# Kernel optimization log

Measured on AMD Instinct MI355X. Metric: run time of the kernel, lower is better.

Reference implementation:

```python
import jax, jax.numpy as jnp
import numpy as np

B, H, S, D = 4, 16, 2048, 64


def setup_inputs() -> dict:
    key = jax.random.key(0)
    kq, kk, kv = jax.random.split(key, 3)
    Q = jax.random.normal(kq, (B, H, S, D), dtype=jnp.float32)
    K = jax.random.normal(kk, (B, H, S, D), dtype=jnp.float32)
    V = jax.random.normal(kv, (B, H, S, D), dtype=jnp.float32)
    # causal mask, True = position is masked (torch.masked_fill semantics)
    mask = jnp.triu(jnp.ones((S, S), dtype=bool), k=1)[None, None, :, :]
    return {"Q": Q, "K": K, "V": V, "mask": mask}


def _custom_softmax(x):
    # Faithful to the source: subtract the GLOBAL max of the tensor,
    # then normalize by the row-sum of exps along the last dim.
    x = x - jnp.max(x)
    e = jnp.exp(x)
    return e / jnp.sum(e, axis=-1, keepdims=True)


def reference(Q, K, V, mask):
    head_dim = jnp.asarray(K.shape[-1], dtype=Q.dtype)
    # scores: [B, H, S_q, S_k]
    scores = jnp.einsum("bhqd,bhkd->bhqk", Q, K) / jnp.sqrt(head_dim)
    scores = jnp.where(mask, -jnp.inf, scores)
    attn = _custom_softmax(scores)
    # p_drop = 0.0 -> dropout branch skipped in original
    out = jnp.einsum("bhqk,bhkd->bhqd", attn, V)
    return out
```

## Files before the change

kernel.cpp:

```cpp
#include <hip/hip_runtime.h>

typedef float    f32x4 __attribute__((ext_vector_type(4)));
typedef _Float16 f16x8 __attribute__((ext_vector_type(8)));

constexpr int S_LEN = 2048;
constexpr int DIM   = 64;
constexpr int QBLK  = 128;
constexpr int KBLK  = 64;

__global__ __launch_bounds__(256, 2)
void fattn(const float* __restrict__ Q, const float* __restrict__ K,
           const float* __restrict__ V, float* __restrict__ Out)
{
    __shared__ _Float16 Ks[2][KBLK * DIM];
    __shared__ _Float16 Vt[2][DIM * KBLK];

    const int tid  = threadIdx.x;
    const int lane = tid & 63;
    const int wv   = tid >> 6;
    const int g    = lane >> 4;
    const int c    = lane & 15;

    const int id   = blockIdx.x;
    const int bh   = (id & 7) * 8 + ((id >> 3) >> 3);
    const int pair = (id >> 3) & 7;
    const size_t base = (size_t)bh * (S_LEN * DIM);

    const int krow = tid >> 3;
    const int kd0  = (tid & 7) * 8;

    const float* Kb = K + base;
    const float* Vb = V + base;

    f32x4 kreg[2][2];
    float vreg[2][8];

#define LOAD_KV(KT)                                                            \
    {                                                                          \
        const int ktb_ = (KT) * KBLK;                                          \
        _Pragma("unroll")                                                      \
        for (int sl = 0; sl < 2; ++sl) {                                       \
            const float* kp = Kb + (size_t)(ktb_ + krow + sl * 32) * DIM + kd0;\
            kreg[sl][0] = *(const f32x4*)kp;                                   \
            kreg[sl][1] = *(const f32x4*)(kp + 4);                             \
            const float* vp = Vb + (size_t)(ktb_ + sl * 32 + wv * 4) * DIM + lane; \
            _Pragma("unroll")                                                  \
            for (int mi = 0; mi < 8; ++mi)                                     \
                vreg[sl][mi] = vp[(size_t)((mi >> 2) * 16 + (mi & 3)) * DIM];  \
        }                                                                      \
    }

#define WRITE_KV(B)                                                            \
    {                                                                          \
        _Pragma("unroll")                                                      \
        for (int sl = 0; sl < 2; ++sl) {                                       \
            const int row = krow + sl * 32;                                    \
            f16x8 kb;                                                          \
            _Pragma("unroll")                                                  \
            for (int i = 0; i < 4; ++i) {                                      \
                kb[i]     = (_Float16)kreg[sl][0][i];                          \
                kb[i + 4] = (_Float16)kreg[sl][1][i];                          \
            }                                                                  \
            *(f16x8*)((char*)Ks[B] + row * 128 + ((kd0 * 2) ^ ((row & 7) << 4))) = kb; \
            f16x8 vb;                                                          \
            _Pragma("unroll")                                                  \
            for (int mi = 0; mi < 8; ++mi) vb[mi] = (_Float16)vreg[sl][mi];    \
            const int oct = wv + sl * 4;                                       \
            *(f16x8*)((char*)Vt[B] + lane * 128 + ((oct * 16) ^ ((lane & 7) << 4))) = vb; \
        }                                                                      \
    }

    #pragma unroll 1
    for (int seg = 0; seg < 2; ++seg) {
        const int qt    = seg ? pair : 15 - pair;
        const int qbase = qt * QBLK;
        const int qw    = qbase + wv * 32;
        const int nkt   = 2 * qt + 2;

        f16x8 qf[2][2];
        #pragma unroll
        for (int qh = 0; qh < 2; ++qh) {
            const float* qp = Q + base + (size_t)(qw + qh * 16 + c) * DIM + g * 8;
            #pragma unroll
            for (int dc = 0; dc < 2; ++dc) {
                const f32x4 f0 = *(const f32x4*)(qp + dc * 32);
                const f32x4 f1 = *(const f32x4*)(qp + dc * 32 + 4);
                f16x8 q;
                #pragma unroll
                for (int i = 0; i < 4; ++i) {
                    q[i]     = (_Float16)(f0[i] * 0.125f);
                    q[i + 4] = (_Float16)(f1[i] * 0.125f);
                }
                qf[dc][qh] = q;
            }
        }

        f32x4 o[4][2];
        #pragma unroll
        for (int dt = 0; dt < 4; ++dt)
            #pragma unroll
            for (int qh = 0; qh < 2; ++qh) o[dt][qh] = (f32x4){0.f, 0.f, 0.f, 0.f};
        float m[2] = {-INFINITY, -INFINITY};
        float l[2] = {0.f, 0.f};

        LOAD_KV(0)
        __syncthreads();
        WRITE_KV(0)
        LOAD_KV(1)
        __syncthreads();

        for (int kt = 0; kt < nkt; ++kt) {
            const int cur = kt & 1;
            const int ktb = kt * KBLK;
            if (kt + 1 < nkt) WRITE_KV(cur ^ 1)
            if (kt + 2 < nkt) LOAD_KV(kt + 2)

            if (ktb <= qw + 31) {
                f32x4 s[4][2];
                __builtin_amdgcn_s_setprio(1);
                #pragma unroll
                for (int ct = 0; ct < 4; ++ct) {
                    const int r = ct * 16 + c;
                    const char* kp = (const char*)Ks[cur] + r * 128;
                    const f16x8 kf0 = *(const f16x8*)(kp + ((g * 16)      ^ ((r & 7) << 4)));
                    const f16x8 kf1 = *(const f16x8*)(kp + ((64 + g * 16) ^ ((r & 7) << 4)));
                    #pragma unroll
                    for (int qh = 0; qh < 2; ++qh) {
                        f32x4 acc = (f32x4){0.f, 0.f, 0.f, 0.f};
                        acc = __builtin_amdgcn_mfma_f32_16x16x32_f16(kf0, qf[0][qh], acc, 0, 0, 0);
                        acc = __builtin_amdgcn_mfma_f32_16x16x32_f16(kf1, qf[1][qh], acc, 0, 0, 0);
                        s[ct][qh] = acc;
                    }
                }
                __builtin_amdgcn_s_setprio(0);

                if (ktb + KBLK - 1 > qw) {
                    #pragma unroll
                    for (int ct = 0; ct < 4; ++ct)
                        #pragma unroll
                        for (int qh = 0; qh < 2; ++qh)
                            #pragma unroll
                            for (int r = 0; r < 4; ++r)
                                if (ktb + ct * 16 + g * 4 + r > qw + qh * 16 + c)
                                    s[ct][qh][r] = -INFINITY;
                }

                float rm[2];
                #pragma unroll
                for (int qh = 0; qh < 2; ++qh) {
                    float v = s[0][qh][0];
                    #pragma unroll
                    for (int ct = 0; ct < 4; ++ct)
                        #pragma unroll
                        for (int r = 0; r < 4; ++r) v = fmaxf(v, s[ct][qh][r]);
                    v = fmaxf(v, __shfl_xor(v, 16));
                    v = fmaxf(v, __shfl_xor(v, 32));
                    rm[qh] = v;
                }
                const float need = fmaxf(rm[0] - m[0], rm[1] - m[1]);
                if (!__all(need <= 8.f)) {
                    #pragma unroll
                    for (int qh = 0; qh < 2; ++qh) {
                        const float mn = fmaxf(m[qh], rm[qh]);
                        const float sc = __expf(m[qh] - mn);
                        m[qh] = mn;
                        l[qh] *= sc;
                        #pragma unroll
                        for (int dt = 0; dt < 4; ++dt)
                            #pragma unroll
                            for (int r = 0; r < 4; ++r) o[dt][qh][r] *= sc;
                    }
                }
                float rs[2] = {0.f, 0.f};
                #pragma unroll
                for (int ct = 0; ct < 4; ++ct)
                    #pragma unroll
                    for (int qh = 0; qh < 2; ++qh)
                        #pragma unroll
                        for (int r = 0; r < 4; ++r) {
                            const float p = __expf(s[ct][qh][r] - m[qh]);
                            s[ct][qh][r] = p;
                            rs[qh] += p;
                        }
                #pragma unroll
                for (int qh = 0; qh < 2; ++qh) {
                    float v = rs[qh];
                    v += __shfl_xor(v, 16);
                    v += __shfl_xor(v, 32);
                    l[qh] += v;
                }

                f16x8 pa[2][2];
                #pragma unroll
                for (int qh = 0; qh < 2; ++qh)
                    #pragma unroll
                    for (int kc = 0; kc < 2; ++kc) {
                        f16x8 p;
                        #pragma unroll
                        for (int r = 0; r < 4; ++r) {
                            p[r]     = (_Float16)s[2 * kc][qh][r];
                            p[r + 4] = (_Float16)s[2 * kc + 1][qh][r];
                        }
                        pa[qh][kc] = p;
                    }

                __builtin_amdgcn_s_setprio(1);
                #pragma unroll
                for (int dt = 0; dt < 4; ++dt) {
                    const int dd = dt * 16 + c;
                    const char* vp = (const char*)Vt[cur] + dd * 128;
                    #pragma unroll
                    for (int kc = 0; kc < 2; ++kc) {
                        const f16x8 vf = *(const f16x8*)(vp +
                            ((kc * 64 + g * 16) ^ ((dd & 7) << 4)));
                        #pragma unroll
                        for (int qh = 0; qh < 2; ++qh)
                            o[dt][qh] = __builtin_amdgcn_mfma_f32_16x16x32_f16(
                                vf, pa[qh][kc], o[dt][qh], 0, 0, 0);
                    }
                }
                __builtin_amdgcn_s_setprio(0);
            }
            __syncthreads();
        }

        #pragma unroll
        for (int qh = 0; qh < 2; ++qh) {
            const float invl = 1.f / l[qh];
            const size_t qoff = base + (size_t)(qw + qh * 16 + c) * DIM;
            #pragma unroll
            for (int dt = 0; dt < 4; ++dt) {
                f32x4 ov;
                #pragma unroll
                for (int r = 0; r < 4; ++r) ov[r] = o[dt][qh][r] * invl;
                *(f32x4*)(Out + qoff + dt * 16 + g * 4) = ov;
            }
        }
    }
#undef LOAD_KV
#undef WRITE_KV
}

extern "C" void kernel_launch(void* const* d_in, const int* in_sizes, int n_in,
                              void* d_out, int out_size, void* d_ws, size_t ws_size,
                              hipStream_t stream)
{
    const float* Q = (const float*)d_in[0];
    const float* K = (const float*)d_in[1];
    const float* V = (const float*)d_in[2];
    float* Out = (float*)d_out;
    fattn<<<dim3(512), 256, 0, stream>>>(Q, K, V, Out);
}
```

Measured before the change: 73.83 us.

## Process paired causal Q tiles concurrently in 512-thread blocks; use exp2 softmax

Each block now has 8 waves. Waves 0-3 handle the heavy query tile and waves 4-7 handle the light mirrored tile, all sharing one K/V stream, so the two segments no longer run one after another. Every thread loads one K/V slice per tile instead of two, which halves per-thread staging registers. Q is prescaled by log2(e)/sqrt(D) so the softmax can use native exp2, and the rescale threshold is raised to match the log2 domain. The light-tile waves sit idle once they pass their causal range but still hit the barrier on every iteration, which adds imbalance and sync cost.

```diff
diff --git a/kernel.cpp b/kernel.cpp
--- a/kernel.cpp
+++ b/kernel.cpp
@@ -8,7 +8,10 @@
 constexpr int QBLK  = 128;
 constexpr int KBLK  = 64;
 
-__global__ __launch_bounds__(256, 2)
+#define QSCALE 0.1803368801111f
+#define THR    11.5f
+
+__global__ __launch_bounds__(512, 4)
 void fattn(const float* __restrict__ Q, const float* __restrict__ K,
            const float* __restrict__ V, float* __restrict__ Out)
 {
@@ -21,220 +24,207 @@
     const int g    = lane >> 4;
     const int c    = lane & 15;
 
-    const int id   = blockIdx.x;
-    const int bh   = (id & 7) * 8 + ((id >> 3) >> 3);
-    const int pair = (id >> 3) & 7;
+    const int id = blockIdx.x;
+    const int bh = (id >> 2) & 63;
+    const int p  = (id & 256) ? (7 - (id & 3)) : (id & 3);
+    const int qt_hi = 15 - p;
+    const int qt = (wv < 4) ? qt_hi : p;
+    const int qw = qt * QBLK + (wv & 3) * 32;
+    const int nkt = 2 * qt_hi + 2;
     const size_t base = (size_t)bh * (S_LEN * DIM);
+
+    f16x8 qf[2][2];
+    #pragma unroll
+    for (int qh = 0; qh < 2; ++qh) {
+        const float* qp = Q + base + (size_t)(qw + qh * 16 + c) * DIM + g * 8;
+        #pragma unroll
+        for (int dc = 0; dc < 2; ++dc) {
+            const f32x4 f0 = *(const f32x4*)(qp + dc * 32);
+            const f32x4 f1 = *(const f32x4*)(qp + dc * 32 + 4);
+            f16x8 q;
+            #pragma unroll
+            for (int i = 0; i < 4; ++i) {
+                q[i]     = (_Float16)(f0[i] * QSCALE);
+                q[i + 4] = (_Float16)(f1[i] * QSCALE);
+            }
+            qf[dc][qh] = q;
+        }
+    }
 
     const int krow = tid >> 3;
     const int kd0  = (tid & 7) * 8;
-
     const float* Kb = K + base;
     const float* Vb = V + base;
-
-    f32x4 kreg[2][2];
-    float vreg[2][8];
+    const int vk0 = (wv >> 2) * 32 + (wv & 3) * 4;
+
+    f32x4 kreg[2];
+    float vreg[8];
 
 #define LOAD_KV(KT)                                                            \
     {                                                                          \
         const int ktb_ = (KT) * KBLK;                                          \
+        const float* kp = Kb + (size_t)(ktb_ + krow) * DIM + kd0;              \
+        kreg[0] = *(const f32x4*)kp;                                           \
+        kreg[1] = *(const f32x4*)(kp + 4);                                     \
+        const float* vp = Vb + (size_t)(ktb_ + vk0) * DIM + lane;              \
         _Pragma("unroll")                                                      \
-        for (int sl = 0; sl < 2; ++sl) {                                       \
-            const float* kp = Kb + (size_t)(ktb_ + krow + sl * 32) * DIM + kd0;\
-            kreg[sl][0] = *(const f32x4*)kp;                                   \
-            kreg[sl][1] = *(const f32x4*)(kp + 4);                             \
-            const float* vp = Vb + (size_t)(ktb_ + sl * 32 + wv * 4) * DIM + lane; \
-            _Pragma("unroll")                                                  \
-            for (int mi = 0; mi < 8; ++mi)                                     \
-                vreg[sl][mi] = vp[(size_t)((mi >> 2) * 16 + (mi & 3)) * DIM];  \
-        }                                                                      \
+        for (int mi = 0; mi < 8; ++mi)                                         \
+            vreg[mi] = vp[(size_t)((mi >> 2) * 16 + (mi & 3)) * DIM];          \
     }
 
 #define WRITE_KV(B)                                                            \
     {                                                                          \
+        f16x8 kb;                                                              \
         _Pragma("unroll")                                                      \
-        for (int sl = 0; sl < 2; ++sl) {                                       \
-            const int row = krow + sl * 32;                                    \
-            f16x8 kb;                                                          \
-            _Pragma("unroll")                                                  \
-            for (int i = 0; i < 4; ++i) {                                      \
-                kb[i]     = (_Float16)kreg[sl][0][i];                          \
-                kb[i + 4] = (_Float16)kreg[sl][1][i];                          \
-            }                                                                  \
-            *(f16x8*)((char*)Ks[B] + row * 128 + ((kd0 * 2) ^ ((row & 7) << 4))) = kb; \
-            f16x8 vb;                                                          \
-            _Pragma("unroll")                                                  \
-            for (int mi = 0; mi < 8; ++mi) vb[mi] = (_Float16)vreg[sl][mi];    \
-            const int oct = wv + sl * 4;                                       \
-            *(f16x8*)((char*)Vt[B] + lane * 128 + ((oct * 16) ^ ((lane & 7) << 4))) = vb; \
+        for (int i = 0; i < 4; ++i) {                                          \
+            kb[i]     = (_Float16)kreg[0][i];                                  \
+            kb[i + 4] = (_Float16)kreg[1][i];                                  \
         }                                                                      \
-    }
-
-    #pragma unroll 1
-    for (int seg = 0; seg < 2; ++seg) {
-        const int qt    = seg ? pair : 15 - pair;
-        const int qbase = qt * QBLK;
-        const int qw    = qbase + wv * 32;
-        const int nkt   = 2 * qt + 2;
-
-        f16x8 qf[2][2];
+        *(f16x8*)((char*)Ks[B] + krow * 128 + ((kd0 * 2) ^ ((krow & 7) << 4))) = kb; \
+        f16x8 vb;                                                              \
+        _Pragma("unroll")                                                      \
+        for (int mi = 0; mi < 8; ++mi) vb[mi] = (_Float16)vreg[mi];            \
+        *(f16x8*)((char*)Vt[B] + lane * 128 + ((wv * 16) ^ ((lane & 7) << 4))) = vb; \
+    }
+
+    f32x4 o[4][2];
+    #pragma unroll
+    for (int dt = 0; dt < 4; ++dt)
         #pragma unroll
-        for (int qh = 0; qh < 2; ++qh) {
-            const float* qp = Q + base + (size_t)(qw + qh * 16 + c) * DIM + g * 8;
-            #pragma unroll
-            for (int dc = 0; dc < 2; ++dc) {
-                const f32x4 f0 = *(const f32x4*)(qp + dc * 32);
-                const f32x4 f1 = *(const f32x4*)(qp + dc * 32 + 4);
-                f16x8 q;
-                #pragma unroll
-                for (int i = 0; i < 4; ++i) {
-                    q[i]     = (_Float16)(f0[i] * 0.125f);
-                    q[i + 4] = (_Float16)(f1[i] * 0.125f);
-                }
-                qf[dc][qh] = q;
-            }
-        }
-
-        f32x4 o[4][2];
-        #pragma unroll
-        for (int dt = 0; dt < 4; ++dt)
-            #pragma unroll
-            for (int qh = 0; qh < 2; ++qh) o[dt][qh] = (f32x4){0.f, 0.f, 0.f, 0.f};
-        float m[2] = {-INFINITY, -INFINITY};
-        float l[2] = {0.f, 0.f};
-
-        LOAD_KV(0)
-        __syncthreads();
-        WRITE_KV(0)
-        LOAD_KV(1)
-        __syncthreads();
-
-        for (int kt = 0; kt < nkt; ++kt) {
-            const int cur = kt & 1;
-            const int ktb = kt * KBLK;
-            if (kt + 1 < nkt) WRITE_KV(cur ^ 1)
-            if (kt + 2 < nkt) LOAD_KV(kt + 2)
-
-            if (ktb <= qw + 31) {
-                f32x4 s[4][2];
-                __builtin_amdgcn_s_setprio(1);
-                #pragma unroll
-                for (int ct = 0; ct < 4; ++ct) {
-                    const int r = ct * 16 + c;
-                    const char* kp = (const char*)Ks[cur] + r * 128;
-                    const f16x8 kf0 = *(const f16x8*)(kp + ((g * 16)      ^ ((r & 7) << 4)));
-                    const f16x8 kf1 = *(const f16x8*)(kp + ((64 + g * 16) ^ ((r & 7) << 4)));
-                    #pragma unroll
-                    for (int qh = 0; qh < 2; ++qh) {
-                        f32x4 acc = (f32x4){0.f, 0.f, 0.f, 0.f};
-                        acc = __builtin_amdgcn_mfma_f32_16x16x32_f16(kf0, qf[0][qh], acc, 0, 0, 0);
-                        acc = __builtin_amdgcn_mfma_f32_16x16x32_f16(kf1, qf[1][qh], acc, 0, 0, 0);
-                        s[ct][qh] = acc;
-                    }
-                }
-                __builtin_amdgcn_s_setprio(0);
-
-                if (ktb + KBLK - 1 > qw) {
-                    #pragma unroll
-                    for (int ct = 0; ct < 4; ++ct)
-                        #pragma unroll
-                        for (int qh = 0; qh < 2; ++qh)
-                            #pragma unroll
-                            for (int r = 0; r < 4; ++r)
-                                if (ktb + ct * 16 + g * 4 + r > qw + qh * 16 + c)
-                                    s[ct][qh][r] = -INFINITY;
-                }
-
-                float rm[2];
+        for (int qh = 0; qh < 2; ++qh) o[dt][qh] = (f32x4){0.f, 0.f, 0.f, 0.f};
+    float m[2] = {-INFINITY, -INFINITY};
+    float l[2] = {0.f, 0.f};
+
+    LOAD_KV(0)
+    WRITE_KV(0)
+    LOAD_KV(1)
+    __syncthreads();
+
+    for (int kt = 0; kt < nkt; ++kt) {
+        const int cur = kt & 1;
+        const int ktb = kt * KBLK;
+        if (kt + 1 < nkt) WRITE_KV(cur ^ 1)
+        if (kt + 2 < nkt) LOAD_KV(kt + 2)
+
+        if (ktb <= qw + 31) {
+            f32x4 s[4][2];
+            __builtin_amdgcn_s_setprio(1);
+            #pragma unroll
+            for (int ct = 0; ct < 4; ++ct) {
+                const int r = ct * 16 + c;
+                const char* kp = (const char*)Ks[cur] + r * 128;
+                const f16x8 kf0 = *(const f16x8*)(kp + ((g * 16)      ^ ((r & 7) << 4)));
+                const f16x8 kf1 = *(const f16x8*)(kp + ((64 + g * 16) ^ ((r & 7) << 4)));
                 #pragma unroll
                 for (int qh = 0; qh < 2; ++qh) {
-                    float v = s[0][qh][0];
-                    #pragma unroll
-                    for (int ct = 0; ct < 4; ++ct)
-                        #pragma unroll
-                        for (int r = 0; r < 4; ++r) v = fmaxf(v, s[ct][qh][r]);
-                    v = fmaxf(v, __shfl_xor(v, 16));
-                    v = fmaxf(v, __shfl_xor(v, 32));
-                    rm[qh] = v;
-                }
-                const float need = fmaxf(rm[0] - m[0], rm[1] - m[1]);
-                if (!__all(need <= 8.f)) {
-                    #pragma unroll
-                    for (int qh = 0; qh < 2; ++qh) {
-                        const float mn = fmaxf(m[qh], rm[qh]);
-                        const float sc = __expf(m[qh] - mn);
-                        m[qh] = mn;
-                        l[qh] *= sc;
-                        #pragma unroll
-                        for (int dt = 0; dt < 4; ++dt)
-                            #pragma unroll
-                            for (int r = 0; r < 4; ++r) o[dt][qh][r] *= sc;
-                    }
-                }
-                float rs[2] = {0.f, 0.f};
+                    f32x4 acc = (f32x4){0.f, 0.f, 0.f, 0.f};
+                    acc = __builtin_amdgcn_mfma_f32_16x16x32_f16(kf0, qf[0][qh], acc, 0, 0, 0);
+                    acc = __builtin_amdgcn_mfma_f32_16x16x32_f16(kf1, qf[1][qh], acc, 0, 0, 0);
+                    s[ct][qh] = acc;
+                }
+            }
+            __builtin_amdgcn_s_setprio(0);
+
+            if (ktb + KBLK - 1 > qw) {
                 #pragma unroll
                 for (int ct = 0; ct < 4; ++ct)
                     #pragma unroll
                     for (int qh = 0; qh < 2; ++qh)
                         #pragma unroll
-                        for (int r = 0; r < 4; ++r) {
-                            const float p = __expf(s[ct][qh][r] - m[qh]);
-                            s[ct][qh][r] = p;
-                            rs[qh] += p;
-                        }
+                        for (int r = 0; r < 4; ++r)
+                            if (ktb + ct * 16 + g * 4 + r > qw + qh * 16 + c)
+                                s[ct][qh][r] = -INFINITY;
+            }
+
+            float rm[2];
+            #pragma unroll
+            for (int qh = 0; qh < 2; ++qh) {
+                float v = s[0][qh][0];
+                #pragma unroll
+                for (int ct = 0; ct < 4; ++ct)
+                    #pragma unroll
+                    for (int r = 0; r < 4; ++r) v = fmaxf(v, s[ct][qh][r]);
+                v = fmaxf(v, __shfl_xor(v, 16));
+                v = fmaxf(v, __shfl_xor(v, 32));
+                rm[qh] = v;
+            }
+            const float need = fmaxf(rm[0] - m[0], rm[1] - m[1]);
+            if (!__all(need <= THR)) {
                 #pragma unroll
                 for (int qh = 0; qh < 2; ++qh) {
-                    float v = rs[qh];
-                    v += __shfl_xor(v, 16);
-                    v += __shfl_xor(v, 32);
-                    l[qh] += v;
-                }
-
-                f16x8 pa[2][2];
+                    const float mn = fmaxf(m[qh], rm[qh]);
+                    const float sc = __builtin_amdgcn_exp2f(m[qh] - mn);
+                    m[qh] = mn;
+                    l[qh] *= sc;
+                    #pragma unroll
+                    for (int dt = 0; dt < 4; ++dt)
+                        #pragma unroll
+                        for (int r = 0; r < 4; ++r) o[dt][qh][r] *= sc;
+                }
+            }
+            float rs[2] = {0.f, 0.f};
+            #pragma unroll
+            for (int ct = 0; ct < 4; ++ct)
                 #pragma unroll
                 for (int qh = 0; qh < 2; ++qh)
                     #pragma unroll
-                    for (int kc = 0; kc < 2; ++kc) {
-                        f16x8 p;
-                        #pragma unroll
-                        for (int r = 0; r < 4; ++r) {
-                            p[r]     = (_Float16)s[2 * kc][qh][r];
-                            p[r + 4] = (_Float16)s[2 * kc + 1][qh][r];
-                        }
-                        pa[qh][kc] = p;
+                    for (int r = 0; r < 4; ++r) {
+                        const float pv = __builtin_amdgcn_exp2f(s[ct][qh][r] - m[qh]);
+                        s[ct][qh][r] = pv;
+                        rs[qh] += pv;
                     }
-
-                __builtin_amdgcn_s_setprio(1);
-                #pragma unroll
-                for (int dt = 0; dt < 4; ++dt) {
-                    const int dd = dt * 16 + c;
-                    const char* vp = (const char*)Vt[cur] + dd * 128;
-                    #pragma unroll
-                    for (int kc = 0; kc < 2; ++kc) {
-                        const f16x8 vf = *(const f16x8*)(vp +
-                            ((kc * 64 + g * 16) ^ ((dd & 7) << 4)));
-                        #pragma unroll
-                        for (int qh = 0; qh < 2; ++qh)
-                            o[dt][qh] = __builtin_amdgcn_mfma_f32_16x16x32_f16(
-                                vf, pa[qh][kc], o[dt][qh], 0, 0, 0);
+            #pragma unroll
+            for (int qh = 0; qh < 2; ++qh) {
+                float v = rs[qh];
+                v += __shfl_xor(v, 16);
+                v += __shfl_xor(v, 32);
+                l[qh] += v;
+            }
+
+            f16x8 pa[2][2];
+            #pragma unroll
+            for (int qh = 0; qh < 2; ++qh)
+                #pragma unroll
+                for (int kc = 0; kc < 2; ++kc) {
+                    f16x8 pk;
+                    #pragma unroll
+                    for (int r = 0; r < 4; ++r) {
+                        pk[r]     = (_Float16)s[2 * kc][qh][r];
+                        pk[r + 4] = (_Float16)s[2 * kc + 1][qh][r];
                     }
-                }
-                __builtin_amdgcn_s_setprio(0);
-            }
-            __syncthreads();
+                    pa[qh][kc] = pk;
+                }
+
+            __builtin_amdgcn_s_setprio(1);
+            #pragma unroll
+            for (int dt = 0; dt < 4; ++dt) {
+                const int dd = dt * 16 + c;
+                const char* vp = (const char*)Vt[cur] + dd * 128;
+                #pragma unroll
+                for (int kc = 0; kc < 2; ++kc) {
+                    const f16x8 vf = *(const f16x8*)(vp +
+                        ((kc * 64 + g * 16) ^ ((dd & 7) << 4)));
+                    #pragma unroll
+                    for (int qh = 0; qh < 2; ++qh)
+                        o[dt][qh] = __builtin_amdgcn_mfma_f32_16x16x32_f16(
+                            vf, pa[qh][kc], o[dt][qh], 0, 0, 0);
+                }
+            }
+            __builtin_amdgcn_s_setprio(0);
         }
-
+        __syncthreads();
+    }
+
+    #pragma unroll
+    for (int qh = 0; qh < 2; ++qh) {
+        const float invl = 1.f / l[qh];
+        const size_t qoff = base + (size_t)(qw + qh * 16 + c) * DIM;
         #pragma unroll
-        for (int qh = 0; qh < 2; ++qh) {
-            const float invl = 1.f / l[qh];
-            const size_t qoff = base + (size_t)(qw + qh * 16 + c) * DIM;
-            #pragma unroll
-            for (int dt = 0; dt < 4; ++dt) {
-                f32x4 ov;
-                #pragma unroll
-                for (int r = 0; r < 4; ++r) ov[r] = o[dt][qh][r] * invl;
-                *(f32x4*)(Out + qoff + dt * 16 + g * 4) = ov;
-            }
+        for (int dt = 0; dt < 4; ++dt) {
+            f32x4 ov;
+            #pragma unroll
+            for (int r = 0; r < 4; ++r) ov[r] = o[dt][qh][r] * invl;
+            *(f32x4*)(Out + qoff + dt * 16 + g * 4) = ov;
         }
     }
 #undef LOAD_KV
@@ -249,5 +239,5 @@
     const float* K = (const float*)d_in[1];
     const float* V = (const float*)d_in[2];
     float* Out = (float*)d_out;
-    fattn<<<dim3(512), 256, 0, stream>>>(Q, K, V, Out);
+    fattn<<<dim3(512), 512, 0, stream>>>(Q, K, V, Out);
 }
```

New measurement: 80.09 us. +8.5%, slower.

## Launch one block per Q tile with heavy tiles first, use exp2 softmax

Applied to the files above, without the earlier changes.

Drops the paired-segment scheme, where each block processed a long and a short causal Q tile in turn. The grid now has 1024 blocks, one Q tile each, ordered so the longest-running tiles are scheduled first, and launch bounds allow 4 blocks per CU instead of 2. Q is pre-scaled by log2(e)/sqrt(d) so the softmax can use the hardware exp2 instruction, and the lazy-rescale threshold is widened to match the base-2 units. The risks are more block scheduling overhead and register pressure from the higher occupancy target, which may cause spills.

```diff
diff --git a/kernel.cpp b/kernel.cpp
--- a/kernel.cpp
+++ b/kernel.cpp
@@ -8,7 +8,10 @@
 constexpr int QBLK  = 128;
 constexpr int KBLK  = 64;
 
-__global__ __launch_bounds__(256, 2)
+#define QSCALE 0.1803368801111f
+#define THR    11.5f
+
+__global__ __launch_bounds__(256, 4)
 void fattn(const float* __restrict__ Q, const float* __restrict__ K,
            const float* __restrict__ V, float* __restrict__ Out)
 {
@@ -21,14 +24,35 @@
     const int g    = lane >> 4;
     const int c    = lane & 15;
 
-    const int id   = blockIdx.x;
-    const int bh   = (id & 7) * 8 + ((id >> 3) >> 3);
-    const int pair = (id >> 3) & 7;
+    const int id    = blockIdx.x;
+    const int local = id >> 3;
+    const int bh    = (id & 7) * 8 + (local & 7);
+    const int qt    = 15 - (local >> 3);
+    const int qbase = qt * QBLK;
+    const int qw    = qbase + wv * 32;
+    const int nkt   = 2 * qt + 2;
     const size_t base = (size_t)bh * (S_LEN * DIM);
+
+    f16x8 qf[2][2];
+    #pragma unroll
+    for (int qh = 0; qh < 2; ++qh) {
+        const float* qp = Q + base + (size_t)(qw + qh * 16 + c) * DIM + g * 8;
+        #pragma unroll
+        for (int dc = 0; dc < 2; ++dc) {
+            const f32x4 f0 = *(const f32x4*)(qp + dc * 32);
+            const f32x4 f1 = *(const f32x4*)(qp + dc * 32 + 4);
+            f16x8 q;
+            #pragma unroll
+            for (int i = 0; i < 4; ++i) {
+                q[i]     = (_Float16)(f0[i] * QSCALE);
+                q[i + 4] = (_Float16)(f1[i] * QSCALE);
+            }
+            qf[dc][qh] = q;
+        }
+    }
 
     const int krow = tid >> 3;
     const int kd0  = (tid & 7) * 8;
-
     const float* Kb = K + base;
     const float* Vb = V + base;
 
@@ -70,171 +94,144 @@
         }                                                                      \
     }
 
-    #pragma unroll 1
-    for (int seg = 0; seg < 2; ++seg) {
-        const int qt    = seg ? pair : 15 - pair;
-        const int qbase = qt * QBLK;
-        const int qw    = qbase + wv * 32;
-        const int nkt   = 2 * qt + 2;
-
-        f16x8 qf[2][2];
+    f32x4 o[4][2];
+    #pragma unroll
+    for (int dt = 0; dt < 4; ++dt)
         #pragma unroll
-        for (int qh = 0; qh < 2; ++qh) {
-            const float* qp = Q + base + (size_t)(qw + qh * 16 + c) * DIM + g * 8;
-            #pragma unroll
-            for (int dc = 0; dc < 2; ++dc) {
-                const f32x4 f0 = *(const f32x4*)(qp + dc * 32);
-                const f32x4 f1 = *(const f32x4*)(qp + dc * 32 + 4);
-                f16x8 q;
-                #pragma unroll
-                for (int i = 0; i < 4; ++i) {
-                    q[i]     = (_Float16)(f0[i] * 0.125f);
-                    q[i + 4] = (_Float16)(f1[i] * 0.125f);
-                }
-                qf[dc][qh] = q;
-            }
-        }
-
-        f32x4 o[4][2];
-        #pragma unroll
-        for (int dt = 0; dt < 4; ++dt)
-            #pragma unroll
-            for (int qh = 0; qh < 2; ++qh) o[dt][qh] = (f32x4){0.f, 0.f, 0.f, 0.f};
-        float m[2] = {-INFINITY, -INFINITY};
-        float l[2] = {0.f, 0.f};
-
-        LOAD_KV(0)
-        __syncthreads();
-        WRITE_KV(0)
-        LOAD_KV(1)
-        __syncthreads();
-
-        for (int kt = 0; kt < nkt; ++kt) {
-            const int cur = kt & 1;
-            const int ktb = kt * KBLK;
-            if (kt + 1 < nkt) WRITE_KV(cur ^ 1)
-            if (kt + 2 < nkt) LOAD_KV(kt + 2)
-
-            if (ktb <= qw + 31) {
-                f32x4 s[4][2];
-                __builtin_amdgcn_s_setprio(1);
-                #pragma unroll
-                for (int ct = 0; ct < 4; ++ct) {
-                    const int r = ct * 16 + c;
-                    const char* kp = (const char*)Ks[cur] + r * 128;
-                    const f16x8 kf0 = *(const f16x8*)(kp + ((g * 16)      ^ ((r & 7) << 4)));
-                    const f16x8 kf1 = *(const f16x8*)(kp + ((64 + g * 16) ^ ((r & 7) << 4)));
-                    #pragma unroll
-                    for (int qh = 0; qh < 2; ++qh) {
-                        f32x4 acc = (f32x4){0.f, 0.f, 0.f, 0.f};
-                        acc = __builtin_amdgcn_mfma_f32_16x16x32_f16(kf0, qf[0][qh], acc, 0, 0, 0);
-                        acc = __builtin_amdgcn_mfma_f32_16x16x32_f16(kf1, qf[1][qh], acc, 0, 0, 0);
-                        s[ct][qh] = acc;
-                    }
-                }
-                __builtin_amdgcn_s_setprio(0);
-
-                if (ktb + KBLK - 1 > qw) {
-                    #pragma unroll
-                    for (int ct = 0; ct < 4; ++ct)
-                        #pragma unroll
-                        for (int qh = 0; qh < 2; ++qh)
-                            #pragma unroll
-                            for (int r = 0; r < 4; ++r)
-                                if (ktb + ct * 16 + g * 4 + r > qw + qh * 16 + c)
-                                    s[ct][qh][r] = -INFINITY;
-                }
-
-                float rm[2];
+        for (int qh = 0; qh < 2; ++qh) o[dt][qh] = (f32x4){0.f, 0.f, 0.f, 0.f};
+    float m[2] = {-INFINITY, -INFINITY};
+    float l[2] = {0.f, 0.f};
+
+    LOAD_KV(0)
+    WRITE_KV(0)
+    LOAD_KV(1)
+    __syncthreads();
+
+    for (int kt = 0; kt < nkt; ++kt) {
+        const int cur = kt & 1;
+        const int ktb = kt * KBLK;
+        if (kt + 1 < nkt) WRITE_KV(cur ^ 1)
+        if (kt + 2 < nkt) LOAD_KV(kt + 2)
+
+        if (ktb <= qw + 31) {
+            f32x4 s[4][2];
+            __builtin_amdgcn_s_setprio(1);
+            #pragma unroll
+            for (int ct = 0; ct < 4; ++ct) {
+                const int r = ct * 16 + c;
+                const char* kp = (const char*)Ks[cur] + r * 128;
+                const f16x8 kf0 = *(const f16x8*)(kp + ((g * 16)      ^ ((r & 7) << 4)));
+                const f16x8 kf1 = *(const f16x8*)(kp + ((64 + g * 16) ^ ((r & 7) << 4)));
                 #pragma unroll
                 for (int qh = 0; qh < 2; ++qh) {
-                    float v = s[0][qh][0];
-                    #pragma unroll
-                    for (int ct = 0; ct < 4; ++ct)
-                        #pragma unroll
-                        for (int r = 0; r < 4; ++r) v = fmaxf(v, s[ct][qh][r]);
-                    v = fmaxf(v, __shfl_xor(v, 16));
-                    v = fmaxf(v, __shfl_xor(v, 32));
-                    rm[qh] = v;
-                }
-                const float need = fmaxf(rm[0] - m[0], rm[1] - m[1]);
-                if (!__all(need <= 8.f)) {
-                    #pragma unroll
-                    for (int qh = 0; qh < 2; ++qh) {
-                        const float mn = fmaxf(m[qh], rm[qh]);
-                        const float sc = __expf(m[qh] - mn);
-                        m[qh] = mn;
-                        l[qh] *= sc;
-                        #pragma unroll
-                        for (int dt = 0; dt < 4; ++dt)
-                            #pragma unroll
-                            for (int r = 0; r < 4; ++r) o[dt][qh][r] *= sc;
-                    }
-                }
-                float rs[2] = {0.f, 0.f};
+                    f32x4 acc = (f32x4){0.f, 0.f, 0.f, 0.f};
+                    acc = __builtin_amdgcn_mfma_f32_16x16x32_f16(kf0, qf[0][qh], acc, 0, 0, 0);
+                    acc = __builtin_amdgcn_mfma_f32_16x16x32_f16(kf1, qf[1][qh], acc, 0, 0, 0);
+                    s[ct][qh] = acc;
+                }
+            }
+            __builtin_amdgcn_s_setprio(0);
+
+            if (ktb + KBLK - 1 > qw) {
                 #pragma unroll
                 for (int ct = 0; ct < 4; ++ct)
                     #pragma unroll
                     for (int qh = 0; qh < 2; ++qh)
                         #pragma unroll
-                        for (int r = 0; r < 4; ++r) {
-                            const float p = __expf(s[ct][qh][r] - m[qh]);
-                            s[ct][qh][r] = p;
-                            rs[qh] += p;
-                        }
+                        for (int r = 0; r < 4; ++r)
+                            if (ktb + ct * 16 + g * 4 + r > qw + qh * 16 + c)
+                                s[ct][qh][r] = -INFINITY;
+            }
+
+            float rm[2];
+            #pragma unroll
+            for (int qh = 0; qh < 2; ++qh) {
+                float v = s[0][qh][0];
+                #pragma unroll
+                for (int ct = 0; ct < 4; ++ct)
+                    #pragma unroll
+                    for (int r = 0; r < 4; ++r) v = fmaxf(v, s[ct][qh][r]);
+                v = fmaxf(v, __shfl_xor(v, 16));
+                v = fmaxf(v, __shfl_xor(v, 32));
+                rm[qh] = v;
+            }
+            const float need = fmaxf(rm[0] - m[0], rm[1] - m[1]);
+            if (!__all(need <= THR)) {
                 #pragma unroll
                 for (int qh = 0; qh < 2; ++qh) {
-                    float v = rs[qh];
-                    v += __shfl_xor(v, 16);
-                    v += __shfl_xor(v, 32);
-                    l[qh] += v;
-                }
-
-                f16x8 pa[2][2];
+                    const float mn = fmaxf(m[qh], rm[qh]);
+                    const float sc = __builtin_amdgcn_exp2f(m[qh] - mn);
+                    m[qh] = mn;
+                    l[qh] *= sc;
+                    #pragma unroll
+                    for (int dt = 0; dt < 4; ++dt)
+                        #pragma unroll
+                        for (int r = 0; r < 4; ++r) o[dt][qh][r] *= sc;
+                }
+            }
+            float rs[2] = {0.f, 0.f};
+            #pragma unroll
+            for (int ct = 0; ct < 4; ++ct)
                 #pragma unroll
                 for (int qh = 0; qh < 2; ++qh)
                     #pragma unroll
-                    for (int kc = 0; kc < 2; ++kc) {
-                        f16x8 p;
-                        #pragma unroll
-                        for (int r = 0; r < 4; ++r) {
-                            p[r]     = (_Float16)s[2 * kc][qh][r];
-                            p[r + 4] = (_Float16)s[2 * kc + 1][qh][r];
-                        }
-                        pa[qh][kc] = p;
+                    for (int r = 0; r < 4; ++r) {
+                        const float pv = __builtin_amdgcn_exp2f(s[ct][qh][r] - m[qh]);
+                        s[ct][qh][r] = pv;
+                        rs[qh] += pv;
                     }
-
-                __builtin_amdgcn_s_setprio(1);
-                #pragma unroll
-                for (int dt = 0; dt < 4; ++dt) {
-                    const int dd = dt * 16 + c;
-                    const char* vp = (const char*)Vt[cur] + dd * 128;
-                    #pragma unroll
-                    for (int kc = 0; kc < 2; ++kc) {
-                        const f16x8 vf = *(const f16x8*)(vp +
-                            ((kc * 64 + g * 16) ^ ((dd & 7) << 4)));
-                        #pragma unroll
-                        for (int qh = 0; qh < 2; ++qh)
-                            o[dt][qh] = __builtin_amdgcn_mfma_f32_16x16x32_f16(
-                                vf, pa[qh][kc], o[dt][qh], 0, 0, 0);
+            #pragma unroll
+            for (int qh = 0; qh < 2; ++qh) {
+                float v = rs[qh];
+                v += __shfl_xor(v, 16);
+                v += __shfl_xor(v, 32);
+                l[qh] += v;
+            }
+
+            f16x8 pa[2][2];
+            #pragma unroll
+            for (int qh = 0; qh < 2; ++qh)
+                #pragma unroll
+                for (int kc = 0; kc < 2; ++kc) {
+                    f16x8 pk;
+                    #pragma unroll
+                    for (int r = 0; r < 4; ++r) {
+                        pk[r]     = (_Float16)s[2 * kc][qh][r];
+                        pk[r + 4] = (_Float16)s[2 * kc + 1][qh][r];
                     }
-                }
-                __builtin_amdgcn_s_setprio(0);
-            }
-            __syncthreads();
+                    pa[qh][kc] = pk;
+                }
+
+            __builtin_amdgcn_s_setprio(1);
+            #pragma unroll
+            for (int dt = 0; dt < 4; ++dt) {
+                const int dd = dt * 16 + c;
+                const char* vp = (const char*)Vt[cur] + dd * 128;
+                #pragma unroll
+                for (int kc = 0; kc < 2; ++kc) {
+                    const f16x8 vf = *(const f16x8*)(vp +
+                        ((kc * 64 + g * 16) ^ ((dd & 7) << 4)));
+                    #pragma unroll
+                    for (int qh = 0; qh < 2; ++qh)
+                        o[dt][qh] = __builtin_amdgcn_mfma_f32_16x16x32_f16(
+                            vf, pa[qh][kc], o[dt][qh], 0, 0, 0);
+                }
+            }
+            __builtin_amdgcn_s_setprio(0);
         }
-
+        __syncthreads();
+    }
+
+    #pragma unroll
+    for (int qh = 0; qh < 2; ++qh) {
+        const float invl = 1.f / l[qh];
+        const size_t qoff = base + (size_t)(qw + qh * 16 + c) * DIM;
         #pragma unroll
-        for (int qh = 0; qh < 2; ++qh) {
-            const float invl = 1.f / l[qh];
-            const size_t qoff = base + (size_t)(qw + qh * 16 + c) * DIM;
-            #pragma unroll
-            for (int dt = 0; dt < 4; ++dt) {
-                f32x4 ov;
-                #pragma unroll
-                for (int r = 0; r < 4; ++r) ov[r] = o[dt][qh][r] * invl;
-                *(f32x4*)(Out + qoff + dt * 16 + g * 4) = ov;
-            }
+        for (int dt = 0; dt < 4; ++dt) {
+            f32x4 ov;
+            #pragma unroll
+            for (int r = 0; r < 4; ++r) ov[r] = o[dt][qh][r] * invl;
+            *(f32x4*)(Out + qoff + dt * 16 + g * 4) = ov;
         }
     }
 #undef LOAD_KV
@@ -249,5 +246,5 @@
     const float* K = (const float*)d_in[1];
     const float* V = (const float*)d_in[2];
     float* Out = (float*)d_out;
-    fattn<<<dim3(512), 256, 0, stream>>>(Q, K, V, Out);
+    fattn<<<dim3(1024), 256, 0, stream>>>(Q, K, V, Out);
 }
```

After: 98.61 us. 1.34x slower.
